# Kernel tuning notes

Measured on AMD Instinct MI355X. Metric: run time of the kernel, lower is better.

Reference implementation:

```python
import jax, jax.numpy as jnp
import numpy as np

NA = 10        # num_agents
P = 65536      # num_parallel envs
IN = 16        # input_size
DP = 2         # dim_p
E = 64         # embed_dim = hidden_dim // 2
H = 128        # h_dim


def _uniform(key, shape):
    # torch init: uniform(-stdv, stdv) with stdv = 1/sqrt(last_dim)
    stdv = 1.0 / np.sqrt(shape[-1])
    return jax.random.uniform(key, shape, jnp.float32, -stdv, stdv)


def setup_inputs() -> dict:
    key = jax.random.key(0)
    ks = jax.random.split(key, 8)
    inp = jax.random.normal(ks[0], (NA * P, IN), jnp.float32)
    W_enc = _uniform(ks[1], (IN - DP, E))
    b_enc = jnp.zeros((E,), jnp.float32)
    W_goal = _uniform(ks[2], (DP, E))
    b_goal = jnp.zeros((E,), jnp.float32)
    Wq = _uniform(ks[3], (E, E))   # n_heads=1, key_dim=val_dim=E
    Wk = _uniform(ks[4], (E, E))
    Wv = _uniform(ks[5], (E, E))
    Wo = _uniform(ks[6], (E, E))
    W_upd = _uniform(ks[7], (2 * E, E))
    b_upd = jnp.zeros((E,), jnp.float32)
    return dict(inp=inp, W_enc=W_enc, b_enc=b_enc, W_goal=W_goal, b_goal=b_goal,
                Wq=Wq, Wk=Wk, Wv=Wv, Wo=Wo, W_upd=W_upd, b_upd=b_upd)


def reference(inp, W_enc, b_enc, W_goal, b_goal, Wq, Wk, Wv, Wo, W_upd, b_upd):
    # split agent features / goal
    agent_inp = inp[:, :IN - DP]                     # (NA*P, 14)
    # goal: view(NA, P, DP).transpose(0,1)[:, 0, :] == first P rows' goal cols
    goal = inp[:P, IN - DP:]                         # (P, DP)

    # encoder: Linear + ReLU, then regroup agent-major -> (P, NA, E)
    h = jax.nn.relu(agent_inp @ W_enc + b_enc)
    h = h.reshape(NA, P, E).transpose(1, 0, 2)       # (P, NA, E)

    # single-head attention with custom mask (eye + first column blocked)
    scale = 1.0 / np.sqrt(E)
    Q = h @ Wq                                       # (P, NA, E)
    K = h @ Wk
    V = h @ Wv
    compat = jnp.einsum('bqd,bkd->bqk', Q, K) * scale  # (P, NA, NA)
    mask = jnp.eye(NA, dtype=bool) | (jnp.arange(NA)[None, :] == 0)
    compat = jnp.where(mask[None, :, :], -jnp.inf, compat)
    attn = jax.nn.softmax(compat, axis=-1)
    m = jnp.einsum('bqk,bkd->bqd', attn, V) @ Wo     # (P, NA, E)

    # update MLP on [h, m]
    h1 = jax.nn.relu(jnp.concatenate([h, m], axis=2) @ W_upd + b_upd)  # (P, NA, E)

    # second half: goal embedding for leader, leader's h for followers
    h2_leader = jax.nn.relu(goal @ W_goal + b_goal)[:, None, :]        # (P, 1, E)
    h2_followers = jnp.broadcast_to(h[:, :1, :], (P, NA - 1, E))        # (P, NA-1, E)
    h2 = jnp.concatenate([h2_leader, h2_followers], axis=1)            # (P, NA, E)

    hc = jnp.concatenate([h1, h2], axis=2)           # (P, NA, H)
    h_leader = hc[:, 0, :]                           # (P, H)
    h_followers = hc[:, 1:, :].transpose(1, 0, 2).reshape(-1, H)  # ((NA-1)*P, H)
    return (h_leader, h_followers)
```

## Files before the change

### kernel.cpp

```cpp
#include <hip/hip_runtime.h>
#include <math.h>

#define NAG 10
#define PP  65536
#define EE  64
#define INW 16
#define TP  4
#define RR  (TP*NAG)
#define SH  72
#define SX  40
#define SOT 132
#define NBLK 1024
#define NGRP (PP/TP)

typedef __attribute__((ext_vector_type(8))) short short8;
typedef __attribute__((ext_vector_type(4))) float f32x4;

__device__ __forceinline__ short f2bf(float x){
    unsigned u = __float_as_uint(x);
    return (short)((u + 0x8000u) >> 16);
}
__device__ __forceinline__ float bf2f(short s){
    return __uint_as_float(((unsigned)(unsigned short)s) << 16);
}

__global__ __launch_bounds__(256, 4) void mpnn_mfma3(
    const float* __restrict__ inp,
    const float* __restrict__ W_enc, const float* __restrict__ b_enc,
    const float* __restrict__ W_goal, const float* __restrict__ b_goal,
    const float* __restrict__ Wq, const float* __restrict__ Wk,
    const float* __restrict__ Wv, const float* __restrict__ Wo,
    const float* __restrict__ W_upd, const float* __restrict__ b_upd,
    float* __restrict__ out)
{
    __shared__ __align__(16) char pool[4 * 48 * SH * 2];
    __shared__ __align__(16) short Xs[48 * SX];
    __shared__ __align__(16) float attn_s[TP][NAG][12];
    __shared__ float goal_s[TP][2];

    short* const hs   = (short*)pool;
    short* const qsb  = hs  + 48*SH;
    short* const ksb  = qsb + 48*SH;
    short* const vsb  = ksb + 48*SH;
    float* const outt = (float*)pool;
    float* const Wc   = (float*)pool;

    const int tid  = threadIdx.x;
    const int w    = tid >> 6;
    const int l    = tid & 63;
    const int lrow = l & 15;
    const int lk   = l >> 4;
    const int col  = 16*w + lrow;

    for (int i = tid; i < EE*EE; i += 256) {
        const int k = i >> 6, n = i & 63;
        float s = 0.f;
        #pragma unroll 8
        for (int d = 0; d < EE; ++d)
            s = fmaf(Wo[k*EE + d], W_upd[(EE + d)*EE + n], s);
        Wc[i] = s;
    }
    __syncthreads();

    short8 fenc, fqw[2], fkw[2], fvw[2], fuw[2], fcw[2];
    #pragma unroll
    for (int j = 0; j < 8; ++j) {
        int k = lk*8 + j;
        fenc[j] = (k < 14) ? f2bf(W_enc[k*EE + col]) : (short)0;
    }
    #pragma unroll
    for (int ks = 0; ks < 2; ++ks) {
        #pragma unroll
        for (int j = 0; j < 8; ++j) {
            int k = 32*ks + lk*8 + j;
            fqw[ks][j] = f2bf(Wq[k*EE + col]);
            fkw[ks][j] = f2bf(Wk[k*EE + col]);
            fvw[ks][j] = f2bf(Wv[k*EE + col]);
            fuw[ks][j] = f2bf(W_upd[k*EE + col]);
            fcw[ks][j] = f2bf(Wc[k*EE + col]);
        }
    }
    const float bencv = b_enc[col];
    const float bupdv = b_upd[col];
    const float wg0 = W_goal[l], wg1 = W_goal[EE + l], bg = b_goal[l];

    for (int i = tid; i < 48*SX; i += 256) Xs[i] = 0;

    const bool hasx = tid < RR*4;
    const int  r_ = tid >> 2, q_ = tid & 3;
    const int  pl_ = r_ / NAG, a_ = r_ - pl_*NAG;
    const size_t xbase = (size_t)a_*PP*INW + (size_t)pl_*INW + (size_t)q_*4;
    f32x4 xin = {0.f,0.f,0.f,0.f};
    if (hasx) xin = __builtin_nontemporal_load(
        (const f32x4*)(inp + xbase + (size_t)blockIdx.x * (TP*INW)));

    for (int g = blockIdx.x; g < NGRP; g += NBLK) {
        const int p0 = g * TP;
        __syncthreads();

        if (hasx) {
            short* xr = &Xs[r_*SX + q_*4];
            xr[0] = f2bf(xin[0]); xr[1] = f2bf(xin[1]);
            if (q_ == 3 && a_ == 0) {
                goal_s[pl_][0] = xin[2]; goal_s[pl_][1] = xin[3];
            } else {
                xr[2] = f2bf(xin[2]); xr[3] = f2bf(xin[3]);
            }
        }
        __syncthreads();

        if (hasx && g + NBLK < NGRP)
            xin = __builtin_nontemporal_load(
                (const f32x4*)(inp + xbase + (size_t)(g + NBLK) * (TP*INW)));

        const float h2l = fmaxf(fmaf(goal_s[w][0], wg0,
                           fmaf(goal_s[w][1], wg1, bg)), 0.f);

        #pragma unroll
        for (int rt = 0; rt < 3; ++rt) {
            const short8 a0 = *reinterpret_cast<const short8*>(&Xs[(16*rt + lrow)*SX + lk*8]);
            f32x4 acc = {0.f,0.f,0.f,0.f};
            acc = __builtin_amdgcn_mfma_f32_16x16x32_bf16(a0, fenc, acc, 0,0,0);
            #pragma unroll
            for (int j = 0; j < 4; ++j)
                hs[(16*rt + lk*4 + j)*SH + col] = f2bf(fmaxf(acc[j] + bencv, 0.f));
        }
        __syncthreads();

        short8 hA0[3], hA1[3];
        #pragma unroll
        for (int rt = 0; rt < 3; ++rt) {
            hA0[rt] = *reinterpret_cast<const short8*>(&hs[(16*rt + lrow)*SH + lk*8]);
            hA1[rt] = *reinterpret_cast<const short8*>(&hs[(16*rt + lrow)*SH + 32 + lk*8]);
            f32x4 qa = {0.f,0.f,0.f,0.f}, ka = {0.f,0.f,0.f,0.f}, va = {0.f,0.f,0.f,0.f};
            qa = __builtin_amdgcn_mfma_f32_16x16x32_bf16(hA0[rt], fqw[0], qa, 0,0,0);
            qa = __builtin_amdgcn_mfma_f32_16x16x32_bf16(hA1[rt], fqw[1], qa, 0,0,0);
            ka = __builtin_amdgcn_mfma_f32_16x16x32_bf16(hA0[rt], fkw[0], ka, 0,0,0);
            ka = __builtin_amdgcn_mfma_f32_16x16x32_bf16(hA1[rt], fkw[1], ka, 0,0,0);
            va = __builtin_amdgcn_mfma_f32_16x16x32_bf16(hA0[rt], fvw[0], va, 0,0,0);
            va = __builtin_amdgcn_mfma_f32_16x16x32_bf16(hA1[rt], fvw[1], va, 0,0,0);
            #pragma unroll
            for (int j = 0; j < 4; ++j) {
                const int ro = (16*rt + lk*4 + j)*SH + col;
                qsb[ro] = f2bf(qa[j]);
                ksb[ro] = f2bf(ka[j]);
                vsb[ro] = f2bf(va[j]);
            }
        }
        const float h0 = bf2f(hs[(w*NAG)*SH + l]);
        __syncthreads();

        {
            const int r0 = w * NAG;
            const short8 aK0 = *reinterpret_cast<const short8*>(&ksb[(r0+lrow)*SH + lk*8]);
            const short8 aK1 = *reinterpret_cast<const short8*>(&ksb[(r0+lrow)*SH + 32 + lk*8]);
            const short8 aQ0 = *reinterpret_cast<const short8*>(&qsb[(r0+lrow)*SH + lk*8]);
            const short8 aQ1 = *reinterpret_cast<const short8*>(&qsb[(r0+lrow)*SH + 32 + lk*8]);
            f32x4 st = {0.f,0.f,0.f,0.f};
            st = __builtin_amdgcn_mfma_f32_16x16x32_bf16(aK0, aQ0, st, 0,0,0);
            st = __builtin_amdgcn_mfma_f32_16x16x32_bf16(aK1, aQ1, st, 0,0,0);
            const int q = lrow;
            float c[4]; float mx4 = -1e30f;
            #pragma unroll
            for (int j = 0; j < 4; ++j) {
                const int k = lk*4 + j;
                const bool valid = (q < NAG) && (k < NAG) && (k != q) && (k != 0);
                c[j] = valid ? st[j] * 0.125f : -1e30f;
                mx4 = fmaxf(mx4, c[j]);
            }
            float mx = fmaxf(mx4, __shfl_xor(mx4, 16, 64));
            mx = fmaxf(mx, __shfl_xor(mx, 32, 64));
            float e[4], s4 = 0.f;
            #pragma unroll
            for (int j = 0; j < 4; ++j) { e[j] = __expf(c[j] - mx); s4 += e[j]; }
            float s = s4;
            s += __shfl_xor(s, 16, 64);
            s += __shfl_xor(s, 32, 64);
            const float inv = 1.f / s;
            if (q < NAG) {
                #pragma unroll
                for (int j = 0; j < 4; ++j) {
                    const int k = lk*4 + j;
                    if (k < NAG) attn_s[w][q][k] = e[j] * inv;
                }
            }

            float vv[NAG];
            #pragma unroll
            for (int kk = 0; kk < NAG; ++kk) vv[kk] = bf2f(vsb[(r0+kk)*SH + l]);
            #pragma unroll
            for (int a = 0; a < NAG; ++a) {
                float m = 0.f;
                #pragma unroll
                for (int t = 0; t < 5; ++t) {
                    const float2 pv = *reinterpret_cast<const float2*>(&attn_s[w][a][2*t]);
                    m = fmaf(pv.x, vv[2*t], fmaf(pv.y, vv[2*t+1], m));
                }
                qsb[(r0+a)*SH + l] = f2bf(m);
            }
        }
        __syncthreads();

        f32x4 uacc[3];
        #pragma unroll
        for (int rt = 0; rt < 3; ++rt) {
            const short8 a2 = *reinterpret_cast<const short8*>(&qsb[(16*rt + lrow)*SH + lk*8]);
            const short8 a3 = *reinterpret_cast<const short8*>(&qsb[(16*rt + lrow)*SH + 32 + lk*8]);
            f32x4 ua = {0.f,0.f,0.f,0.f};
            ua = __builtin_amdgcn_mfma_f32_16x16x32_bf16(hA0[rt], fuw[0], ua, 0,0,0);
            ua = __builtin_amdgcn_mfma_f32_16x16x32_bf16(hA1[rt], fuw[1], ua, 0,0,0);
            ua = __builtin_amdgcn_mfma_f32_16x16x32_bf16(a2,      fcw[0], ua, 0,0,0);
            ua = __builtin_amdgcn_mfma_f32_16x16x32_bf16(a3,      fcw[1], ua, 0,0,0);
            uacc[rt] = ua;
        }
        __syncthreads();

        #pragma unroll
        for (int rt = 0; rt < 3; ++rt) {
            #pragma unroll
            for (int j = 0; j < 4; ++j) {
                const int r = 16*rt + lk*4 + j;
                if (r < RR) outt[r*SOT + col] = fmaxf(uacc[rt][j] + bupdv, 0.f);
            }
        }
        outt[(w*NAG)*SOT + 64 + l] = h2l;
        #pragma unroll
        for (int a = 1; a < NAG; ++a)
            outt[(w*NAG + a)*SOT + 64 + l] = h0;
        __syncthreads();

        float* __restrict__ outF = out + (size_t)PP*128;
        #pragma unroll
        for (int it = 0; it < 5; ++it) {
            const int flat   = it*256 + tid;
            const int a      = flat >> 7;
            const int within = flat & 127;
            const int pl     = within >> 5;
            const int j4     = within & 31;
            const f32x4 v = *reinterpret_cast<const f32x4*>(&outt[(pl*NAG + a)*SOT + j4*4]);
            float* dst = (a == 0)
                ? (out  + ((size_t)(p0 + pl))*128 + j4*4)
                : (outF + ((size_t)(a-1)*PP + (size_t)(p0 + pl))*128 + j4*4);
            __builtin_nontemporal_store(v, (f32x4*)dst);
        }
    }
}

extern "C" void kernel_launch(void* const* d_in, const int* in_sizes, int n_in,
                              void* d_out, int out_size, void* d_ws, size_t ws_size,
                              hipStream_t stream) {
    const float* inp    = (const float*)d_in[0];
    const float* W_enc  = (const float*)d_in[1];
    const float* b_enc  = (const float*)d_in[2];
    const float* W_goal = (const float*)d_in[3];
    const float* b_goal = (const float*)d_in[4];
    const float* Wq     = (const float*)d_in[5];
    const float* Wk     = (const float*)d_in[6];
    const float* Wv     = (const float*)d_in[7];
    const float* Wo     = (const float*)d_in[8];
    const float* W_upd  = (const float*)d_in[9];
    const float* b_upd  = (const float*)d_in[10];

    hipLaunchKernelGGL(mpnn_mfma3, dim3(NBLK), dim3(256), 0, stream,
                       inp, W_enc, b_enc, W_goal, b_goal,
                       Wq, Wk, Wv, Wo, W_upd, b_upd, (float*)d_out);
}
```

Baseline: 255.0 us.

## Restructure MPNN kernel: MFMA attention-V product, separate output staging, higher occupancy

The attention-weighted V product now runs on a 16x16x16 bf16 MFMA using a transposed V buffer, replacing the scalar FMA loop and the attn_s shared array. The output staging tile is split into an update part and a compact h2 part that holds one goal row and one leader row per env, so LDS use shrinks and the h/qsb fragments are reloaded from LDS instead of kept in registers. These savings allow 5 blocks per CU and a grid of 1280 blocks. The write of the next input into Xs is folded into an existing barrier, which drops two syncthreads per iteration, and Xs packing uses 64-bit stores. In exchange there are extra LDS reads and a bf16 rounding of attention probabilities.

```diff
diff --git a/kernel.cpp b/kernel.cpp
--- a/kernel.cpp
+++ b/kernel.cpp
@@ -9,12 +9,20 @@
 #define RR  (TP*NAG)
 #define SH  72
 #define SX  40
-#define SOT 132
-#define NBLK 1024
+#define SVT 52
+#define SU  68
+#define NBLK 1280
 #define NGRP (PP/TP)
 
 typedef __attribute__((ext_vector_type(8))) short short8;
+typedef __attribute__((ext_vector_type(4))) short short4v;
 typedef __attribute__((ext_vector_type(4))) float f32x4;
+
+#if defined(__has_builtin)
+#if __has_builtin(__builtin_amdgcn_mfma_f32_16x16x16bf16_1k)
+#define HAVE_MFMA16 1
+#endif
+#endif
 
 __device__ __forceinline__ short f2bf(float x){
     unsigned u = __float_as_uint(x);
@@ -23,8 +31,11 @@
 __device__ __forceinline__ float bf2f(short s){
     return __uint_as_float(((unsigned)(unsigned short)s) << 16);
 }
-
-__global__ __launch_bounds__(256, 4) void mpnn_mfma3(
+__device__ __forceinline__ unsigned pack2(float a, float b){
+    return (unsigned)(unsigned short)f2bf(a) | ((unsigned)(unsigned short)f2bf(b) << 16);
+}
+
+__global__ __launch_bounds__(256, 5) void mpnn_mfma4(
     const float* __restrict__ inp,
     const float* __restrict__ W_enc, const float* __restrict__ b_enc,
     const float* __restrict__ W_goal, const float* __restrict__ b_goal,
@@ -33,17 +44,20 @@
     const float* __restrict__ W_upd, const float* __restrict__ b_upd,
     float* __restrict__ out)
 {
-    __shared__ __align__(16) char pool[4 * 48 * SH * 2];
+    __shared__ __align__(16) char pool[27392];
     __shared__ __align__(16) short Xs[48 * SX];
-    __shared__ __align__(16) float attn_s[TP][NAG][12];
     __shared__ float goal_s[TP][2];
+#ifndef HAVE_MFMA16
+    __shared__ float attn_s[TP][NAG][12];
+#endif
 
     short* const hs   = (short*)pool;
     short* const qsb  = hs  + 48*SH;
     short* const ksb  = qsb + 48*SH;
-    short* const vsb  = ksb + 48*SH;
-    float* const outt = (float*)pool;
-    float* const Wc   = (float*)pool;
+    short* const vsbT = ksb + 48*SH;
+    float* const Wc     = (float*)pool;
+    float* const outt_u = (float*)(pool + 2*2*48*SH);
+    float* const outt_h = (float*)(pool + 2*2*48*SH) + RR*SU;
 
     const int tid  = threadIdx.x;
     const int w    = tid >> 6;
@@ -51,6 +65,8 @@
     const int lrow = l & 15;
     const int lk   = l >> 4;
     const int col  = 16*w + lrow;
+
+    for (int i = tid; i < 48*SX; i += 256) Xs[i] = 0;
 
     for (int i = tid; i < EE*EE; i += 256) {
         const int k = i >> 6, n = i & 63;
@@ -84,8 +100,6 @@
     const float bupdv = b_upd[col];
     const float wg0 = W_goal[l], wg1 = W_goal[EE + l], bg = b_goal[l];
 
-    for (int i = tid; i < 48*SX; i += 256) Xs[i] = 0;
-
     const bool hasx = tid < RR*4;
     const int  r_ = tid >> 2, q_ = tid & 3;
     const int  pl_ = r_ / NAG, a_ = r_ - pl_*NAG;
@@ -94,58 +108,52 @@
     if (hasx) xin = __builtin_nontemporal_load(
         (const f32x4*)(inp + xbase + (size_t)blockIdx.x * (TP*INW)));
 
+    if (hasx) {
+        uint2 pk = { pack2(xin[0], xin[1]), pack2(xin[2], xin[3]) };
+        *(uint2*)&Xs[r_*SX + q_*4] = pk;
+        if (q_ == 3 && a_ == 0) { goal_s[pl_][0] = xin[2]; goal_s[pl_][1] = xin[3]; }
+        if ((int)blockIdx.x + NBLK < NGRP)
+            xin = __builtin_nontemporal_load(
+                (const f32x4*)(inp + xbase + (size_t)(blockIdx.x + NBLK) * (TP*INW)));
+    }
+    __syncthreads();
+
     for (int g = blockIdx.x; g < NGRP; g += NBLK) {
         const int p0 = g * TP;
-        __syncthreads();
-
-        if (hasx) {
-            short* xr = &Xs[r_*SX + q_*4];
-            xr[0] = f2bf(xin[0]); xr[1] = f2bf(xin[1]);
-            if (q_ == 3 && a_ == 0) {
-                goal_s[pl_][0] = xin[2]; goal_s[pl_][1] = xin[3];
-            } else {
-                xr[2] = f2bf(xin[2]); xr[3] = f2bf(xin[3]);
-            }
-        }
-        __syncthreads();
-
-        if (hasx && g + NBLK < NGRP)
-            xin = __builtin_nontemporal_load(
-                (const f32x4*)(inp + xbase + (size_t)(g + NBLK) * (TP*INW)));
 
         const float h2l = fmaxf(fmaf(goal_s[w][0], wg0,
                            fmaf(goal_s[w][1], wg1, bg)), 0.f);
 
         #pragma unroll
         for (int rt = 0; rt < 3; ++rt) {
-            const short8 a0 = *reinterpret_cast<const short8*>(&Xs[(16*rt + lrow)*SX + lk*8]);
+            const short8 ax = *reinterpret_cast<const short8*>(&Xs[(16*rt + lrow)*SX + lk*8]);
             f32x4 acc = {0.f,0.f,0.f,0.f};
-            acc = __builtin_amdgcn_mfma_f32_16x16x32_bf16(a0, fenc, acc, 0,0,0);
+            acc = __builtin_amdgcn_mfma_f32_16x16x32_bf16(ax, fenc, acc, 0,0,0);
             #pragma unroll
             for (int j = 0; j < 4; ++j)
                 hs[(16*rt + lk*4 + j)*SH + col] = f2bf(fmaxf(acc[j] + bencv, 0.f));
         }
         __syncthreads();
 
-        short8 hA0[3], hA1[3];
         #pragma unroll
         for (int rt = 0; rt < 3; ++rt) {
-            hA0[rt] = *reinterpret_cast<const short8*>(&hs[(16*rt + lrow)*SH + lk*8]);
-            hA1[rt] = *reinterpret_cast<const short8*>(&hs[(16*rt + lrow)*SH + 32 + lk*8]);
+            const short8 a0 = *reinterpret_cast<const short8*>(&hs[(16*rt + lrow)*SH + lk*8]);
+            const short8 a1 = *reinterpret_cast<const short8*>(&hs[(16*rt + lrow)*SH + 32 + lk*8]);
             f32x4 qa = {0.f,0.f,0.f,0.f}, ka = {0.f,0.f,0.f,0.f}, va = {0.f,0.f,0.f,0.f};
-            qa = __builtin_amdgcn_mfma_f32_16x16x32_bf16(hA0[rt], fqw[0], qa, 0,0,0);
-            qa = __builtin_amdgcn_mfma_f32_16x16x32_bf16(hA1[rt], fqw[1], qa, 0,0,0);
-            ka = __builtin_amdgcn_mfma_f32_16x16x32_bf16(hA0[rt], fkw[0], ka, 0,0,0);
-            ka = __builtin_amdgcn_mfma_f32_16x16x32_bf16(hA1[rt], fkw[1], ka, 0,0,0);
-            va = __builtin_amdgcn_mfma_f32_16x16x32_bf16(hA0[rt], fvw[0], va, 0,0,0);
-            va = __builtin_amdgcn_mfma_f32_16x16x32_bf16(hA1[rt], fvw[1], va, 0,0,0);
+            qa = __builtin_amdgcn_mfma_f32_16x16x32_bf16(a0, fqw[0], qa, 0,0,0);
+            qa = __builtin_amdgcn_mfma_f32_16x16x32_bf16(a1, fqw[1], qa, 0,0,0);
+            ka = __builtin_amdgcn_mfma_f32_16x16x32_bf16(a0, fkw[0], ka, 0,0,0);
+            ka = __builtin_amdgcn_mfma_f32_16x16x32_bf16(a1, fkw[1], ka, 0,0,0);
+            va = __builtin_amdgcn_mfma_f32_16x16x32_bf16(a0, fvw[0], va, 0,0,0);
+            va = __builtin_amdgcn_mfma_f32_16x16x32_bf16(a1, fvw[1], va, 0,0,0);
             #pragma unroll
             for (int j = 0; j < 4; ++j) {
                 const int ro = (16*rt + lk*4 + j)*SH + col;
                 qsb[ro] = f2bf(qa[j]);
                 ksb[ro] = f2bf(ka[j]);
-                vsb[ro] = f2bf(va[j]);
-            }
+            }
+            uint2 vpk = { pack2(va[0], va[1]), pack2(va[2], va[3]) };
+            *(uint2*)&vsbT[col*SVT + 16*rt + lk*4] = vpk;
         }
         const float h0 = bf2f(hs[(w*NAG)*SH + l]);
         __syncthreads();
@@ -177,6 +185,28 @@
             s += __shfl_xor(s, 16, 64);
             s += __shfl_xor(s, 32, 64);
             const float inv = 1.f / s;
+
+#ifdef HAVE_MFMA16
+            short4v pa;
+            #pragma unroll
+            for (int j = 0; j < 4; ++j) pa[j] = f2bf(e[j] * inv);
+            #pragma unroll
+            for (int t = 0; t < 4; ++t) {
+                const short* vp = &vsbT[(16*t + lrow)*SVT + r0 + lk*4];
+                const unsigned lo = *(const unsigned*)(vp);
+                const unsigned hi = *(const unsigned*)(vp + 2);
+                short4v vb;
+                vb[0] = (short)(lo & 0xffff); vb[1] = (short)(lo >> 16);
+                vb[2] = (short)(hi & 0xffff); vb[3] = (short)(hi >> 16);
+                f32x4 md = {0.f,0.f,0.f,0.f};
+                md = __builtin_amdgcn_mfma_f32_16x16x16bf16_1k(pa, vb, md, 0,0,0);
+                #pragma unroll
+                for (int j = 0; j < 4; ++j) {
+                    const int a = lk*4 + j;
+                    if (a < NAG) qsb[(r0+a)*SH + 16*t + lrow] = f2bf(md[j]);
+                }
+            }
+#else
             if (q < NAG) {
                 #pragma unroll
                 for (int j = 0; j < 4; ++j) {
@@ -184,49 +214,48 @@
                     if (k < NAG) attn_s[w][q][k] = e[j] * inv;
                 }
             }
-
             float vv[NAG];
             #pragma unroll
-            for (int kk = 0; kk < NAG; ++kk) vv[kk] = bf2f(vsb[(r0+kk)*SH + l]);
+            for (int kk = 0; kk < NAG; ++kk) vv[kk] = bf2f(vsbT[l*SVT + r0 + kk]);
             #pragma unroll
             for (int a = 0; a < NAG; ++a) {
                 float m = 0.f;
                 #pragma unroll
-                for (int t = 0; t < 5; ++t) {
-                    const float2 pv = *reinterpret_cast<const float2*>(&attn_s[w][a][2*t]);
-                    m = fmaf(pv.x, vv[2*t], fmaf(pv.y, vv[2*t+1], m));
-                }
+                for (int kk = 0; kk < NAG; ++kk)
+                    m = fmaf(attn_s[w][a][kk], vv[kk], m);
                 qsb[(r0+a)*SH + l] = f2bf(m);
             }
-        }
-        __syncthreads();
-
-        f32x4 uacc[3];
+#endif
+        }
+        if (hasx && g + NBLK < NGRP) {
+            uint2 pk = { pack2(xin[0], xin[1]), pack2(xin[2], xin[3]) };
+            *(uint2*)&Xs[r_*SX + q_*4] = pk;
+            if (q_ == 3 && a_ == 0) { goal_s[pl_][0] = xin[2]; goal_s[pl_][1] = xin[3]; }
+            if (g + 2*NBLK < NGRP)
+                xin = __builtin_nontemporal_load(
+                    (const f32x4*)(inp + xbase + (size_t)(g + 2*NBLK) * (TP*INW)));
+        }
+        __syncthreads();
+
         #pragma unroll
         for (int rt = 0; rt < 3; ++rt) {
+            const short8 a0 = *reinterpret_cast<const short8*>(&hs [(16*rt + lrow)*SH + lk*8]);
+            const short8 a1 = *reinterpret_cast<const short8*>(&hs [(16*rt + lrow)*SH + 32 + lk*8]);
             const short8 a2 = *reinterpret_cast<const short8*>(&qsb[(16*rt + lrow)*SH + lk*8]);
             const short8 a3 = *reinterpret_cast<const short8*>(&qsb[(16*rt + lrow)*SH + 32 + lk*8]);
             f32x4 ua = {0.f,0.f,0.f,0.f};
-            ua = __builtin_amdgcn_mfma_f32_16x16x32_bf16(hA0[rt], fuw[0], ua, 0,0,0);
-            ua = __builtin_amdgcn_mfma_f32_16x16x32_bf16(hA1[rt], fuw[1], ua, 0,0,0);
-            ua = __builtin_amdgcn_mfma_f32_16x16x32_bf16(a2,      fcw[0], ua, 0,0,0);
-            ua = __builtin_amdgcn_mfma_f32_16x16x32_bf16(a3,      fcw[1], ua, 0,0,0);
-            uacc[rt] = ua;
-        }
-        __syncthreads();
-
-        #pragma unroll
-        for (int rt = 0; rt < 3; ++rt) {
+            ua = __builtin_amdgcn_mfma_f32_16x16x32_bf16(a0, fuw[0], ua, 0,0,0);
+            ua = __builtin_amdgcn_mfma_f32_16x16x32_bf16(a1, fuw[1], ua, 0,0,0);
+            ua = __builtin_amdgcn_mfma_f32_16x16x32_bf16(a2, fcw[0], ua, 0,0,0);
+            ua = __builtin_amdgcn_mfma_f32_16x16x32_bf16(a3, fcw[1], ua, 0,0,0);
             #pragma unroll
             for (int j = 0; j < 4; ++j) {
                 const int r = 16*rt + lk*4 + j;
-                if (r < RR) outt[r*SOT + col] = fmaxf(uacc[rt][j] + bupdv, 0.f);
-            }
-        }
-        outt[(w*NAG)*SOT + 64 + l] = h2l;
-        #pragma unroll
-        for (int a = 1; a < NAG; ++a)
-            outt[(w*NAG + a)*SOT + 64 + l] = h0;
+                if (r < RR) outt_u[r*SU + col] = fmaxf(ua[j] + bupdv, 0.f);
+            }
+        }
+        outt_h[(w*2 + 0)*64 + l] = h2l;
+        outt_h[(w*2 + 1)*64 + l] = h0;
         __syncthreads();
 
         float* __restrict__ outF = out + (size_t)PP*128;
@@ -237,7 +266,10 @@
             const int within = flat & 127;
             const int pl     = within >> 5;
             const int j4     = within & 31;
-            const f32x4 v = *reinterpret_cast<const f32x4*>(&outt[(pl*NAG + a)*SOT + j4*4]);
+            const float* src = (j4 < 16)
+                ? &outt_u[(pl*NAG + a)*SU + j4*4]
+                : &outt_h[(pl*2 + (a == 0 ? 0 : 1))*64 + (j4 - 16)*4];
+            const f32x4 v = *reinterpret_cast<const f32x4*>(src);
             float* dst = (a == 0)
                 ? (out  + ((size_t)(p0 + pl))*128 + j4*4)
                 : (outF + ((size_t)(a-1)*PP + (size_t)(p0 + pl))*128 + j4*4);
@@ -261,7 +293,7 @@
     const float* W_upd  = (const float*)d_in[9];
     const float* b_upd  = (const float*)d_in[10];
 
-    hipLaunchKernelGGL(mpnn_mfma3, dim3(NBLK), dim3(256), 0, stream,
+    hipLaunchKernelGGL(mpnn_mfma4, dim3(NBLK), dim3(256), 0, stream,
                        inp, W_enc, b_enc, W_goal, b_goal,
                        Wq, Wk, Wv, Wo, W_upd, b_upd, (float*)d_out);
 }
```

Result: slower. 261.5 us (+2.6%).
